# Performance work log

Hardware: AMD Instinct MI355X
Metric: run time of the kernel (lower is better)

The kernel has to match this reference:

```python
import jax, jax.numpy as jnp
import numpy as np

WORD_NUM = 8
LAYER_NUM = 1
N, D = 8192, 256
V, LLM_DIM = 20000, 4096


def setup_inputs() -> dict:
    key = jax.random.key(0)
    k1, k2, k3, k4, k5 = jax.random.split(key, 5)
    return {
        "z_e": jax.random.normal(k1, (N, D), dtype=jnp.float32),
        "codebook_pca": jax.random.normal(k2, (V, LLM_DIM), dtype=jnp.float32),
        "W_map": jax.random.normal(k3, (D, LLM_DIM), dtype=jnp.float32) * (1.0 / np.sqrt(LLM_DIM)),
        "b_map": jax.random.normal(k4, (D,), dtype=jnp.float32) * 0.01,
        "token_id": jax.random.randint(k5, (V,), 0, 32000, dtype=jnp.int64) if jax.config.jax_enable_x64 else jax.random.randint(k5, (V,), 0, 32000).astype(jnp.int32),
    }


def reference(z_e, codebook_pca, W_map, b_map, token_id):
    sg = jax.lax.stop_gradient
    # codebook_mapping: Linear(llm_dim -> codebook_dim)
    mapped = codebook_pca @ W_map.T + b_map          # (V, D)
    cb_sq = jnp.sum(mapped * mapped, axis=1)          # (V,)
    n, d = z_e.shape
    B = n // WORD_NUM
    z_q = jnp.zeros_like(z_e)
    vq_loss = jnp.float32(0.0)
    commitment_loss = jnp.float32(0.0)
    tensor_indices = None
    token_to_quantize = None
    for i in range(LAYER_NUM):
        residual = z_e - z_q                           # (N, D)
        # squared euclidean distances via ||r||^2 + ||c||^2 - 2 r.c
        dist = (jnp.sum(residual * residual, axis=1, keepdims=True)
                + cb_sq
                - 2.0 * (residual @ mapped.T))         # (N, V)
        dist = dist.reshape(B, WORD_NUM, -1)           # (B, W, V)
        idx_per_word = []
        col = jnp.arange(dist.shape[-1])
        for j in range(WORD_NUM):  # greedy: pick best for word j, mask that code for the whole group
            idx_j = jnp.argmin(dist[:, j, :], axis=1)  # (B,)
            idx_per_word.append(idx_j)
            mask = col[None, :] == idx_j[:, None]      # (B, V)
            dist = jnp.where(mask[:, None, :], jnp.inf, dist)
        flat_idx = jnp.stack(idx_per_word, axis=1).reshape(-1)  # (N,)
        z_q = z_q + mapped[flat_idx]
        vq_loss = vq_loss + jnp.mean((z_q - sg(z_e)) ** 2)
        commitment_loss = commitment_loss + jnp.mean((z_e - sg(z_q)) ** 2)
        if i == 0:
            tensor_indices = flat_idx[:, None]          # (N, 1)
            token_to_quantize = residual[:, None, :]    # (N, 1, D)
    z_q_st = z_e + sg(z_q - z_e)  # straight-through estimator
    loss = 0.75 * vq_loss + 0.25 * commitment_loss
    return z_q_st, loss, token_id[tensor_indices], token_to_quantize
```

## Files before the change

kernel.cpp:

```cpp
#include <hip/hip_runtime.h>
#include <cstdint>
#include <cstddef>

#define N_ROWS 8192
#define DIM    256
#define VCB    20000
#define LLM    4096
#define NCHUNK 16
#define TILES2 157

#define OFF_MAPPED   0ull
#define OFF_CBSQ     5120000ull
#define OFF_PARTD    5140032ull
#define OFF_PARTI    7237184ull
#define OFF_MERGED_D 9334336ull
#define OFF_MERGED_I 9465408ull
#define OFF_FLAT     9596480ull
#define OFF_LOSSP    9604672ull

#define OUT0_OFF 0ull
#define LOSS_OFF 2097152ull
#define OUT2_OFF 2097153ull
#define OUT3_OFF 2105345ull

__device__ __forceinline__ void topk_insert(float s, int idx, float (&td)[16], int (&ti)[16]) {
  bool gate = (s < td[15]) || (s == td[15] && idx < ti[15]);
  if (gate) {
    float cd = s; int ci = idx;
#pragma unroll
    for (int q = 0; q < 16; ++q) {
      bool less = (cd < td[q]) || (cd == td[q] && ci < ti[q]);
      float od = td[q]; int oi = ti[q];
      if (less) { td[q] = cd; ti[q] = ci; cd = od; ci = oi; }
    }
  }
}

__global__ __launch_bounds__(256, 3) void gemm1_kernel(
    const float* __restrict__ A, const float* __restrict__ Wm,
    const float* __restrict__ bmap, float* __restrict__ mapped) {
  __shared__ float As[128][33];
  __shared__ float Bs[128][33];
  const int tid = threadIdx.x;
  const int ty = tid >> 4, tx = tid & 15;
  const int v0 = blockIdx.x * 128;
  const int d0 = blockIdx.y * 128;
  float acc[8][8];
#pragma unroll
  for (int i = 0; i < 8; ++i)
#pragma unroll
    for (int j = 0; j < 8; ++j) acc[i][j] = 0.f;

  for (int kc = 0; kc < LLM / 32; ++kc) {
    const int k0 = kc * 32;
    __syncthreads();
#pragma unroll
    for (int t4 = 0; t4 < 4; ++t4) {
      int f = tid + t4 * 256;
      int r = f >> 3;
      int c4 = (f & 7) << 2;
      int av = v0 + r; av = av < VCB ? av : VCB - 1;
      float4 qa = *reinterpret_cast<const float4*>(A + (size_t)av * LLM + k0 + c4);
      As[r][c4 + 0] = qa.x; As[r][c4 + 1] = qa.y; As[r][c4 + 2] = qa.z; As[r][c4 + 3] = qa.w;
      float4 qb = *reinterpret_cast<const float4*>(Wm + (size_t)(d0 + r) * LLM + k0 + c4);
      Bs[r][c4 + 0] = qb.x; Bs[r][c4 + 1] = qb.y; Bs[r][c4 + 2] = qb.z; Bs[r][c4 + 3] = qb.w;
    }
    __syncthreads();
#pragma unroll 4
    for (int kk = 0; kk < 32; ++kk) {
      float za[8], mb[8];
#pragma unroll
      for (int i = 0; i < 8; ++i) za[i] = As[ty * 8 + i][kk];
#pragma unroll
      for (int j = 0; j < 8; ++j) mb[j] = Bs[tx * 8 + j][kk];
#pragma unroll
      for (int i = 0; i < 8; ++i)
#pragma unroll
        for (int j = 0; j < 8; ++j) acc[i][j] = fmaf(za[i], mb[j], acc[i][j]);
    }
  }
#pragma unroll
  for (int i = 0; i < 8; ++i) {
    int v = v0 + ty * 8 + i;
    if (v < VCB) {
#pragma unroll
      for (int j = 0; j < 8; ++j) {
        int d = d0 + tx * 8 + j;
        mapped[(size_t)v * DIM + d] = acc[i][j] + bmap[d];
      }
    }
  }
}

__global__ void cbsq_kernel(const float* __restrict__ mapped, float* __restrict__ cbsq) {
  const int lane = threadIdx.x & 63;
  const int wid = threadIdx.x >> 6;
  const int row = blockIdx.x * 4 + wid;
  float s = 0.f;
#pragma unroll
  for (int e = 0; e < 4; ++e) {
    float x = mapped[(size_t)row * DIM + lane + e * 64];
    s += x * x;
  }
#pragma unroll
  for (int off = 32; off > 0; off >>= 1) s += __shfl_down(s, off, 64);
  if (lane == 0) cbsq[row] = s;
}

__global__ __launch_bounds__(256, 3) void dist_topk_kernel(
    const float* __restrict__ z_e, const float* __restrict__ mapped,
    const float* __restrict__ cbsq, float* __restrict__ part_d, int* __restrict__ part_i) {
  __shared__ float zs[128][33];
  __shared__ float ms[128][33];
  __shared__ float ss[128][33];
  __shared__ float cbs[128];
  const int tid = threadIdx.x;
  const int ty = tid >> 4, tx = tid & 15;
  const int r0 = blockIdx.x * 128;
  const int chunk = blockIdx.y;

  float topd[16]; int topi[16];
#pragma unroll
  for (int q = 0; q < 16; ++q) { topd[q] = __builtin_inff(); topi[q] = 0x7fffffff; }

  for (int t = chunk; t < TILES2; t += NCHUNK) {
    const int c0 = t * 128;
    float acc[8][8];
#pragma unroll
    for (int i = 0; i < 8; ++i)
#pragma unroll
      for (int j = 0; j < 8; ++j) acc[i][j] = 0.f;

    for (int kc = 0; kc < 8; ++kc) {
      __syncthreads();
      if (kc == 0 && tid < 128) {
        int gc = c0 + tid;
        cbs[tid] = (gc < VCB) ? cbsq[gc] : __builtin_inff();
      }
      const int k0 = kc * 32;
#pragma unroll
      for (int t4 = 0; t4 < 4; ++t4) {
        int f = tid + t4 * 256;
        int r = f >> 3;
        int c4 = (f & 7) << 2;
        float4 qz = *reinterpret_cast<const float4*>(z_e + (size_t)(r0 + r) * DIM + k0 + c4);
        zs[r][c4 + 0] = qz.x; zs[r][c4 + 1] = qz.y; zs[r][c4 + 2] = qz.z; zs[r][c4 + 3] = qz.w;
        int cc = c0 + r; cc = cc < VCB ? cc : VCB - 1;
        float4 qm = *reinterpret_cast<const float4*>(mapped + (size_t)cc * DIM + k0 + c4);
        ms[r][c4 + 0] = qm.x; ms[r][c4 + 1] = qm.y; ms[r][c4 + 2] = qm.z; ms[r][c4 + 3] = qm.w;
      }
      __syncthreads();
#pragma unroll 4
      for (int kk = 0; kk < 32; ++kk) {
        float za[8], mb[8];
#pragma unroll
        for (int i = 0; i < 8; ++i) za[i] = zs[ty * 8 + i][kk];
#pragma unroll
        for (int j = 0; j < 8; ++j) mb[j] = ms[tx * 8 + j][kk];
#pragma unroll
        for (int i = 0; i < 8; ++i)
#pragma unroll
          for (int j = 0; j < 8; ++j) acc[i][j] = fmaf(za[i], mb[j], acc[i][j]);
      }
    }
#pragma unroll
    for (int g = 0; g < 4; ++g) {
      __syncthreads();
      if ((tx >> 2) == g) {
        const int txl = tx & 3;
#pragma unroll
        for (int i = 0; i < 8; ++i)
#pragma unroll
          for (int j = 0; j < 8; ++j)
            ss[ty * 8 + i][txl * 8 + j] = cbs[tx * 8 + j] - 2.0f * acc[i][j];
      }
      __syncthreads();
      if (tid < 128) {
        const int cbase = c0 + g * 32;
#pragma unroll 1
        for (int c = 0; c < 32; ++c) {
          int gc = cbase + c;
          if (gc < VCB) {
            float s = ss[tid][c];
            topk_insert(s, gc, topd, topi);
          }
        }
      }
    }
  }
  if (tid < 128) {
    const size_t row = (size_t)(r0 + tid);
    const size_t base = (row * NCHUNK + chunk) * 16;
#pragma unroll
    for (int q = 0; q < 16; ++q) { part_d[base + q] = topd[q]; part_i[base + q] = topi[q]; }
  }
}

__global__ void merge_kernel(const float* __restrict__ part_d, const int* __restrict__ part_i,
                             float* __restrict__ md, int* __restrict__ mi) {
  const int row = blockIdx.x * blockDim.x + threadIdx.x;
  if (row >= N_ROWS) return;
  float topd[16]; int topi[16];
#pragma unroll
  for (int q = 0; q < 16; ++q) { topd[q] = __builtin_inff(); topi[q] = 0x7fffffff; }
  const float* pd = part_d + (size_t)row * (NCHUNK * 16);
  const int* pi = part_i + (size_t)row * (NCHUNK * 16);
#pragma unroll 1
  for (int c = 0; c < NCHUNK * 16; ++c) topk_insert(pd[c], pi[c], topd, topi);
#pragma unroll
  for (int q = 0; q < 16; ++q) {
    md[(size_t)row * 16 + q] = topd[q];
    mi[(size_t)row * 16 + q] = topi[q];
  }
}

__global__ void select_kernel(const int* __restrict__ mi, int* __restrict__ flat) {
  const int g = blockIdx.x * blockDim.x + threadIdx.x;
  if (g >= N_ROWS / 8) return;
  int banned[8];
#pragma unroll
  for (int j = 0; j < 8; ++j) {
    const int row = g * 8 + j;
    const int* cand = mi + (size_t)row * 16;
    int pick = -1;
#pragma unroll
    for (int s = 0; s < 16; ++s) {
      int c = cand[s];
      bool bad = false;
#pragma unroll
      for (int b = 0; b < 8; ++b)
        if (b < j) bad = bad || (banned[b] == c);
      if (pick < 0 && !bad) pick = c;
    }
    banned[j] = pick;
    flat[row] = pick;
  }
}

__global__ void output_kernel(const float* __restrict__ z_e, const float* __restrict__ mapped,
                              const int* __restrict__ flat, const int* __restrict__ token_id,
                              float* __restrict__ out, float* __restrict__ lossp) {
  const int d = threadIdx.x;
  const int r0 = blockIdx.x * 8;
  float lsum = 0.f;
  float* out0 = out + OUT0_OFF;
  float* out2 = out + OUT2_OFF;
  float* out3 = out + OUT3_OFF;
#pragma unroll 1
  for (int q = 0; q < 8; ++q) {
    const int row = r0 + q;
    const int idx = flat[row];
    float m = mapped[(size_t)idx * DIM + d];
    float ze = z_e[(size_t)row * DIM + d];
    float diff = m - ze;
    out0[(size_t)row * DIM + d] = ze + diff;
    out3[(size_t)row * DIM + d] = ze;
    lsum += diff * diff;
    if (d == 0) out2[row] = (float)token_id[idx];
  }
  __shared__ float red[256];
  red[threadIdx.x] = lsum;
  __syncthreads();
  for (int off = 128; off > 0; off >>= 1) {
    if (threadIdx.x < off) red[threadIdx.x] += red[threadIdx.x + off];
    __syncthreads();
  }
  if (threadIdx.x == 0) lossp[blockIdx.x] = red[0];
}

__global__ void loss_kernel(const float* __restrict__ lossp, float* __restrict__ out) {
  __shared__ float red[256];
  float s = 0.f;
  for (int i = threadIdx.x; i < 1024; i += 256) s += lossp[i];
  red[threadIdx.x] = s;
  __syncthreads();
  for (int off = 128; off > 0; off >>= 1) {
    if (threadIdx.x < off) red[threadIdx.x] += red[threadIdx.x + off];
    __syncthreads();
  }
  if (threadIdx.x == 0) out[LOSS_OFF] = red[0] * (1.0f / 2097152.0f);
}

extern "C" void kernel_launch(void* const* d_in, const int* in_sizes, int n_in,
                              void* d_out, int out_size, void* d_ws, size_t ws_size,
                              hipStream_t stream) {
  const float* z_e      = (const float*)d_in[0];
  const float* codebook = (const float*)d_in[1];
  const float* Wm       = (const float*)d_in[2];
  const float* bmap     = (const float*)d_in[3];
  const int*   token_id = (const int*)d_in[4];

  float* ws     = (float*)d_ws;
  float* mapped = ws + OFF_MAPPED;
  float* cbsq   = ws + OFF_CBSQ;
  float* part_d = ws + OFF_PARTD;
  int*   part_i = (int*)(ws + OFF_PARTI);
  float* md     = ws + OFF_MERGED_D;
  int*   mi     = (int*)(ws + OFF_MERGED_I);
  int*   flat   = (int*)(ws + OFF_FLAT);
  float* lossp  = ws + OFF_LOSSP;
  float* out    = (float*)d_out;

  gemm1_kernel<<<dim3(TILES2, 2), 256, 0, stream>>>(codebook, Wm, bmap, mapped);
  cbsq_kernel<<<VCB / 4, 256, 0, stream>>>(mapped, cbsq);
  dist_topk_kernel<<<dim3(N_ROWS / 128, NCHUNK), 256, 0, stream>>>(z_e, mapped, cbsq, part_d, part_i);
  merge_kernel<<<N_ROWS / 256, 256, 0, stream>>>(part_d, part_i, md, mi);
  select_kernel<<<4, 256, 0, stream>>>(mi, flat);
  output_kernel<<<N_ROWS / 8, 256, 0, stream>>>(z_e, mapped, flat, token_id, out, lossp);
  loss_kernel<<<1, 256, 0, stream>>>(lossp, out);
}
```

Measured before the change: 5.199 ms.

## Restructure GEMM shared-memory tiles for float4 LDS reads and strided thread mapping

Both GEMM kernels now pad shared tiles to a stride of 36 and store global float4 loads directly. The inner products read float4 along k, with threads mapped to rows and columns strided by 16, which replaces scalar, bank-conflicted LDS reads. gemm1 shrinks its V tile to 64 to launch more blocks at higher occupancy and hoists the bias loads. dist_topk reuses the zs buffer for the score staging tile to cut LDS use, at the cost of extra barriers and a different tile-to-thread mapping.

```diff
diff --git a/kernel.cpp b/kernel.cpp
--- a/kernel.cpp
+++ b/kernel.cpp
@@ -36,18 +36,23 @@
   }
 }
 
-__global__ __launch_bounds__(256, 3) void gemm1_kernel(
+__global__ __launch_bounds__(256, 4) void gemm1_kernel(
     const float* __restrict__ A, const float* __restrict__ Wm,
     const float* __restrict__ bmap, float* __restrict__ mapped) {
-  __shared__ float As[128][33];
-  __shared__ float Bs[128][33];
+  __shared__ float As[64][36];
+  __shared__ float Bs[128][36];
   const int tid = threadIdx.x;
   const int ty = tid >> 4, tx = tid & 15;
-  const int v0 = blockIdx.x * 128;
+  const int v0 = blockIdx.x * 64;
   const int d0 = blockIdx.y * 128;
-  float acc[8][8];
-#pragma unroll
-  for (int i = 0; i < 8; ++i)
+
+  float bv[8];
+#pragma unroll
+  for (int j = 0; j < 8; ++j) bv[j] = bmap[d0 + j * 16 + tx];
+
+  float acc[4][8];
+#pragma unroll
+  for (int i = 0; i < 4; ++i)
 #pragma unroll
     for (int j = 0; j < 8; ++j) acc[i][j] = 0.f;
 
@@ -55,39 +60,49 @@
     const int k0 = kc * 32;
     __syncthreads();
 #pragma unroll
-    for (int t4 = 0; t4 < 4; ++t4) {
-      int f = tid + t4 * 256;
+    for (int t = 0; t < 2; ++t) {
+      int f = tid + t * 256;
       int r = f >> 3;
       int c4 = (f & 7) << 2;
       int av = v0 + r; av = av < VCB ? av : VCB - 1;
-      float4 qa = *reinterpret_cast<const float4*>(A + (size_t)av * LLM + k0 + c4);
-      As[r][c4 + 0] = qa.x; As[r][c4 + 1] = qa.y; As[r][c4 + 2] = qa.z; As[r][c4 + 3] = qa.w;
-      float4 qb = *reinterpret_cast<const float4*>(Wm + (size_t)(d0 + r) * LLM + k0 + c4);
-      Bs[r][c4 + 0] = qb.x; Bs[r][c4 + 1] = qb.y; Bs[r][c4 + 2] = qb.z; Bs[r][c4 + 3] = qb.w;
-    }
-    __syncthreads();
-#pragma unroll 4
-    for (int kk = 0; kk < 32; ++kk) {
-      float za[8], mb[8];
-#pragma unroll
-      for (int i = 0; i < 8; ++i) za[i] = As[ty * 8 + i][kk];
-#pragma unroll
-      for (int j = 0; j < 8; ++j) mb[j] = Bs[tx * 8 + j][kk];
-#pragma unroll
-      for (int i = 0; i < 8; ++i)
-#pragma unroll
-        for (int j = 0; j < 8; ++j) acc[i][j] = fmaf(za[i], mb[j], acc[i][j]);
-    }
-  }
-#pragma unroll
-  for (int i = 0; i < 8; ++i) {
-    int v = v0 + ty * 8 + i;
+      *reinterpret_cast<float4*>(&As[r][c4]) =
+          *reinterpret_cast<const float4*>(A + (size_t)av * LLM + k0 + c4);
+    }
+#pragma unroll
+    for (int t = 0; t < 4; ++t) {
+      int f = tid + t * 256;
+      int r = f >> 3;
+      int c4 = (f & 7) << 2;
+      *reinterpret_cast<float4*>(&Bs[r][c4]) =
+          *reinterpret_cast<const float4*>(Wm + (size_t)(d0 + r) * LLM + k0 + c4);
+    }
+    __syncthreads();
+#pragma unroll
+    for (int q = 0; q < 8; ++q) {
+      float4 za[4];
+#pragma unroll
+      for (int i = 0; i < 4; ++i)
+        za[i] = *reinterpret_cast<const float4*>(&As[i * 16 + ty][q * 4]);
+#pragma unroll
+      for (int j = 0; j < 8; ++j) {
+        float4 mb = *reinterpret_cast<const float4*>(&Bs[j * 16 + tx][q * 4]);
+#pragma unroll
+        for (int i = 0; i < 4; ++i) {
+          acc[i][j] = fmaf(za[i].x, mb.x, acc[i][j]);
+          acc[i][j] = fmaf(za[i].y, mb.y, acc[i][j]);
+          acc[i][j] = fmaf(za[i].z, mb.z, acc[i][j]);
+          acc[i][j] = fmaf(za[i].w, mb.w, acc[i][j]);
+        }
+      }
+    }
+  }
+#pragma unroll
+  for (int i = 0; i < 4; ++i) {
+    int v = v0 + i * 16 + ty;
     if (v < VCB) {
 #pragma unroll
-      for (int j = 0; j < 8; ++j) {
-        int d = d0 + tx * 8 + j;
-        mapped[(size_t)v * DIM + d] = acc[i][j] + bmap[d];
-      }
+      for (int j = 0; j < 8; ++j)
+        mapped[(size_t)v * DIM + d0 + j * 16 + tx] = acc[i][j] + bv[j];
     }
   }
 }
@@ -110,10 +125,11 @@
 __global__ __launch_bounds__(256, 3) void dist_topk_kernel(
     const float* __restrict__ z_e, const float* __restrict__ mapped,
     const float* __restrict__ cbsq, float* __restrict__ part_d, int* __restrict__ part_i) {
-  __shared__ float zs[128][33];
-  __shared__ float ms[128][33];
-  __shared__ float ss[128][33];
+  __shared__ float zs[128][36];
+  __shared__ float ms[128][36];
   __shared__ float cbs[128];
+  float (*ss)[33] = reinterpret_cast<float(*)[33]>(&zs[0][0]);
+
   const int tid = threadIdx.x;
   const int ty = tid >> 4, tx = tid & 15;
   const int r0 = blockIdx.x * 128;
@@ -143,36 +159,42 @@
         int f = tid + t4 * 256;
         int r = f >> 3;
         int c4 = (f & 7) << 2;
-        float4 qz = *reinterpret_cast<const float4*>(z_e + (size_t)(r0 + r) * DIM + k0 + c4);
-        zs[r][c4 + 0] = qz.x; zs[r][c4 + 1] = qz.y; zs[r][c4 + 2] = qz.z; zs[r][c4 + 3] = qz.w;
+        *reinterpret_cast<float4*>(&zs[r][c4]) =
+            *reinterpret_cast<const float4*>(z_e + (size_t)(r0 + r) * DIM + k0 + c4);
         int cc = c0 + r; cc = cc < VCB ? cc : VCB - 1;
-        float4 qm = *reinterpret_cast<const float4*>(mapped + (size_t)cc * DIM + k0 + c4);
-        ms[r][c4 + 0] = qm.x; ms[r][c4 + 1] = qm.y; ms[r][c4 + 2] = qm.z; ms[r][c4 + 3] = qm.w;
+        *reinterpret_cast<float4*>(&ms[r][c4]) =
+            *reinterpret_cast<const float4*>(mapped + (size_t)cc * DIM + k0 + c4);
       }
       __syncthreads();
-#pragma unroll 4
-      for (int kk = 0; kk < 32; ++kk) {
-        float za[8], mb[8];
-#pragma unroll
-        for (int i = 0; i < 8; ++i) za[i] = zs[ty * 8 + i][kk];
-#pragma unroll
-        for (int j = 0; j < 8; ++j) mb[j] = ms[tx * 8 + j][kk];
+#pragma unroll
+      for (int q = 0; q < 8; ++q) {
+        float4 za[8];
 #pragma unroll
         for (int i = 0; i < 8; ++i)
-#pragma unroll
-          for (int j = 0; j < 8; ++j) acc[i][j] = fmaf(za[i], mb[j], acc[i][j]);
-      }
-    }
+          za[i] = *reinterpret_cast<const float4*>(&zs[i * 16 + ty][q * 4]);
+#pragma unroll
+        for (int j = 0; j < 8; ++j) {
+          float4 mb = *reinterpret_cast<const float4*>(&ms[j * 16 + tx][q * 4]);
+#pragma unroll
+          for (int i = 0; i < 8; ++i) {
+            acc[i][j] = fmaf(za[i].x, mb.x, acc[i][j]);
+            acc[i][j] = fmaf(za[i].y, mb.y, acc[i][j]);
+            acc[i][j] = fmaf(za[i].z, mb.z, acc[i][j]);
+            acc[i][j] = fmaf(za[i].w, mb.w, acc[i][j]);
+          }
+        }
+      }
+    }
+    __syncthreads();
 #pragma unroll
     for (int g = 0; g < 4; ++g) {
-      __syncthreads();
-      if ((tx >> 2) == g) {
-        const int txl = tx & 3;
-#pragma unroll
-        for (int i = 0; i < 8; ++i)
-#pragma unroll
-          for (int j = 0; j < 8; ++j)
-            ss[ty * 8 + i][txl * 8 + j] = cbs[tx * 8 + j] - 2.0f * acc[i][j];
+#pragma unroll
+      for (int i = 0; i < 8; ++i) {
+#pragma unroll
+        for (int jj = 0; jj < 2; ++jj) {
+          const int j = g * 2 + jj;
+          ss[i * 16 + ty][jj * 16 + tx] = cbs[j * 16 + tx] - 2.0f * acc[i][j];
+        }
       }
       __syncthreads();
       if (tid < 128) {
@@ -180,12 +202,10 @@
 #pragma unroll 1
         for (int c = 0; c < 32; ++c) {
           int gc = cbase + c;
-          if (gc < VCB) {
-            float s = ss[tid][c];
-            topk_insert(s, gc, topd, topi);
-          }
+          if (gc < VCB) topk_insert(ss[tid][c], gc, topd, topi);
         }
       }
+      __syncthreads();
     }
   }
   if (tid < 128) {
@@ -301,7 +321,7 @@
   float* lossp  = ws + OFF_LOSSP;
   float* out    = (float*)d_out;
 
-  gemm1_kernel<<<dim3(TILES2, 2), 256, 0, stream>>>(codebook, Wm, bmap, mapped);
+  gemm1_kernel<<<dim3((VCB + 63) / 64, 2), 256, 0, stream>>>(codebook, Wm, bmap, mapped);
   cbsq_kernel<<<VCB / 4, 256, 0, stream>>>(mapped, cbsq);
   dist_topk_kernel<<<dim3(N_ROWS / 128, NCHUNK), 256, 0, stream>>>(z_e, mapped, cbsq, part_d, part_i);
   merge_kernel<<<N_ROWS / 256, 256, 0, stream>>>(part_d, part_i, md, mi);
```

After: 5.491 ms. 5.6% more time.
